# Kernel tuning notes

Measured on AMD Instinct MI355X. Metric: run time of the kernel, lower is better.

## Reference

```python
import jax, jax.numpy as jnp
import numpy as np

B, D_IN, H, C, K, ND = 65536, 1024, 512, 2, 4, 7
LN_EPS = 1e-5
CE_W = jnp.array([0.1, 0.9], dtype=jnp.float32)


def setup_inputs() -> dict:
    key = jax.random.key(0)
    ks = jax.random.split(key, 12)
    x = jax.random.normal(ks[0], (B, D_IN), dtype=jnp.float32)
    labels = jax.random.randint(ks[1], (B,), 0, C)
    domain = jax.random.randint(ks[2], (B,), 0, ND)
    fc1_w = jax.random.normal(ks[3], (120, D_IN), dtype=jnp.float32) / np.sqrt(D_IN)
    fc1_b = jnp.zeros((120,), dtype=jnp.float32)
    fc2_w = jax.random.normal(ks[4], (H, 120), dtype=jnp.float32) / np.sqrt(120)
    fc2_b = jnp.zeros((H,), dtype=jnp.float32)
    ln_g = jnp.ones((H,), dtype=jnp.float32)
    ln_b = jnp.zeros((H,), dtype=jnp.float32)
    sms = 0.1 * jax.random.normal(ks[5], (K + 1, H, C), dtype=jnp.float32)
    sm_biases = 0.1 * jax.random.normal(ks[6], (K + 1, C), dtype=jnp.float32)
    embs = 1e-4 * jax.random.normal(ks[7], (ND, K), dtype=jnp.float32)
    cs_wt = jnp.asarray(0.1, dtype=jnp.float32) + 1e-4 * jax.random.normal(ks[8], (), dtype=jnp.float32)
    return {"x": x, "labels": labels, "domain": domain, "fc1_w": fc1_w, "fc1_b": fc1_b,
            "fc2_w": fc2_w, "fc2_b": fc2_b, "ln_g": ln_g, "ln_b": ln_b,
            "sms": sms, "sm_biases": sm_biases, "embs": embs, "cs_wt": cs_wt}


def _weighted_ce(logits, labels, w):
    # torch CrossEntropyLoss(weight=w): sum_i w[y_i]*nll_i / sum_i w[y_i]
    logp = jax.nn.log_softmax(logits, axis=-1)
    nll = -jnp.take_along_axis(logp, labels[:, None], axis=1)[:, 0]
    wl = w[labels]
    return jnp.sum(wl * nll) / jnp.sum(wl)


def reference(x, labels, domain, fc1_w, fc1_b, fc2_w, fc2_b, ln_g, ln_b, sms, sm_biases, embs, cs_wt):
    h = jax.nn.relu(x @ fc1_w.T + fc1_b)           # [B,120]
    h = jax.nn.relu(h @ fc2_w.T + fc2_b)           # [B,H]
    mu = jnp.mean(h, axis=-1, keepdims=True)
    var = jnp.var(h, axis=-1, keepdims=True)
    h = (h - mu) / jnp.sqrt(var + LN_EPS) * ln_g + ln_b

    # common classifier (expert 0)
    logits_common = h @ sms[0] + sm_biases[0]      # [B,C]

    # domain mixture weights
    dom1h = jax.nn.one_hot(domain, ND, dtype=jnp.float32)
    c_wts = dom1h @ embs                           # [B,K]
    c_wts = jnp.tanh(jnp.concatenate([jnp.full((h.shape[0], 1), 1.0, jnp.float32) * cs_wt, c_wts], axis=1))  # [B,K+1]

    # reordered einsum chain: K+1 small GEMMs then weighted sum (avoids [B,K+1,H] weight tensor)
    per_k = jnp.einsum('bh,khc->bkc', h, sms)      # [B,K+1,C]
    logits_spec = jnp.einsum('bk,bkc->bc', c_wts, per_k) + c_wts @ sm_biases  # [B,C]

    specific_loss = _weighted_ce(logits_spec, labels, CE_W)
    class_loss = _weighted_ce(logits_common, labels, CE_W)

    # orthogonality penalty: per-class gram of expert weight columns vs identity
    cps = jnp.einsum('khc,jhc->ckj', sms, sms)     # [C,K+1,K+1]
    orth_loss = jnp.mean((cps - jnp.eye(K + 1, dtype=jnp.float32)[None]) ** 2)

    loss = class_loss + specific_loss + orth_loss
    return (loss, logits_common, class_loss, specific_loss, orth_loss)
```

## Files before the change

### kernel.cpp

```cpp
#include <hip/hip_runtime.h>
#include <hip/hip_bf16.h>

typedef __attribute__((ext_vector_type(8))) short short8;
typedef __attribute__((ext_vector_type(4))) float floatx4;
typedef __attribute__((ext_vector_type(8))) unsigned short ushort8;

#define BTOT 65536
#define WS_W1BF   0u
#define WS_W2BF   262144u
#define WS_GBF    393216u
#define WS_CONST  409600u
#define WS_H1BF   524288u
#define WS_PART   17301504u

__device__ __forceinline__ unsigned short f2bf(float f) {
  unsigned u = __float_as_uint(f);
  unsigned r = u + 0x7FFFu + ((u >> 16) & 1u);
  return (unsigned short)(r >> 16);
}

__device__ __forceinline__ unsigned cvtpk(float lo, float hi) {
  unsigned r;
  asm("v_cvt_pk_bf16_f32 %0, %1, %2" : "=v"(r) : "v"(lo), "v"(hi));
  return r;
}

__device__ __forceinline__ void gload16(const void* g, void* l) {
  __builtin_amdgcn_global_load_lds(
      (const __attribute__((address_space(1))) unsigned int*)g,
      (__attribute__((address_space(3))) unsigned int*)l, 16, 0, 0);
}

__global__ __launch_bounds__(256) void k0_prep(
    const float* __restrict__ w1, const float* __restrict__ w2,
    const float* __restrict__ ln_g, const float* __restrict__ ln_b,
    const float* __restrict__ sms, const float* __restrict__ smb,
    const float* __restrict__ embs, const float* __restrict__ cs,
    unsigned char* __restrict__ ws) {
  const int blk = blockIdx.x, tid = threadIdx.x;
  if (blk < 32) {
    for (int g = blk * 256 + tid; g < 16384; g += 32 * 256) {
      int ks = g >> 10, d = g & 1023;
      int n = d >> 3, cp = d & 7, c = cp ^ (n & 7);
      ushort8 u;
      if (n < 120) {
        const float* s = w1 + n * 1024 + ks * 64 + c * 8;
        float4 v0 = *(const float4*)s, v1 = *(const float4*)(s + 4);
        u[0] = f2bf(v0.x); u[1] = f2bf(v0.y); u[2] = f2bf(v0.z); u[3] = f2bf(v0.w);
        u[4] = f2bf(v1.x); u[5] = f2bf(v1.y); u[6] = f2bf(v1.z); u[7] = f2bf(v1.w);
      } else {
#pragma unroll
        for (int j = 0; j < 8; ++j) u[j] = 0;
      }
      *(ushort8*)(ws + WS_W1BF + (unsigned)g * 16) = u;
    }
  } else if (blk < 40) {
    for (int g = (blk - 32) * 256 + tid; g < 8192; g += 8 * 256) {
      int lane = g & 63, f = g >> 6;
      int nt = f & 3, ks = (f >> 2) & 3, w = f >> 4;
      int n = w * 64 + nt * 16 + (lane & 15);
      ushort8 u;
#pragma unroll
      for (int j = 0; j < 8; ++j) {
        int khat = ks * 32 + (lane >> 4) * 8 + j;
        int kcol = (khat & 7) * 16 + (khat >> 3);
        u[j] = (kcol < 120) ? f2bf(w2[n * 120 + kcol]) : (unsigned short)0;
      }
      *(ushort8*)(ws + WS_W2BF + (unsigned)g * 16) = u;
    }
  } else if (blk == 40) {
    for (int e = tid; e < 1024; e += 256) {
      int t = e >> 6, lane = e & 63, q = lane & 15;
      ushort8 u;
#pragma unroll
      for (int j = 0; j < 8; ++j) {
        int khat = t * 32 + (lane >> 4) * 8 + j;
        int col = (khat >> 6) * 64 + (khat & 3) * 16 + ((khat >> 2) & 15);
        float v = 0.f;
        if (q < 10) { int kk = q >> 1, c = q & 1; v = ln_g[col] * sms[kk * 1024 + col * 2 + c]; }
        u[j] = f2bf(v);
      }
      *(ushort8*)(ws + WS_GBF + (unsigned)e * 16) = u;
    }
  } else {
    float* cst = (float*)(ws + WS_CONST);
    int lane = tid & 63, w = tid >> 6;
    for (int q = w; q < 10; q += 4) {
      int kk = q >> 1, c = q & 1;
      float s = 0.f;
#pragma unroll
      for (int i = 0; i < 8; ++i) { int k = lane + 64 * i; s += ln_b[k] * sms[kk * 1024 + k * 2 + c]; }
#pragma unroll
      for (int o = 32; o >= 1; o >>= 1) s += __shfl_xor(s, o);
      if (lane == 0) cst[q] = s + smb[kk * 2 + c];
    }
    if (tid == 0) cst[16] = tanhf(cs[0]);
    if (tid < 28) cst[32 + tid] = tanhf(embs[tid]);
  }
}

__global__ __launch_bounds__(512, 4) void k1_gemm1(
    const float* __restrict__ x, const unsigned char* __restrict__ w1bf,
    const float* __restrict__ b1, unsigned char* __restrict__ h1bf) {
  __shared__ unsigned char lds[32768];
  const int tid = threadIdx.x, lane = tid & 63, w = tid >> 6;
  const int l15 = lane & 15, l4 = lane >> 4;

  float b1v[8];
#pragma unroll
  for (int nt = 0; nt < 8; ++nt) {
    int col = nt * 16 + l15;
    b1v[nt] = b1[col < 120 ? col : 119];
  }
  __builtin_amdgcn_sched_barrier(0);

  const float* xbase = x + ((long)blockIdx.x * 128 + w * 16 + l15) * 1024 + l4 * 8;
  const unsigned char* wsrc = w1bf + w * 2048 + lane * 16;

  floatx4 acc[8];
#pragma unroll
  for (int i = 0; i < 8; ++i) acc[i] = floatx4{0.f, 0.f, 0.f, 0.f};

  float4 p[2][4];
  gload16(wsrc, lds + w * 2048);
  gload16(wsrc + 1024, lds + w * 2048 + 1024);
  __builtin_amdgcn_sched_barrier(0);
#pragma unroll
  for (int ss = 0; ss < 2; ++ss) {
    p[0][ss * 2]     = *(const float4*)(xbase + ss * 32);
    p[0][ss * 2 + 1] = *(const float4*)(xbase + ss * 32 + 4);
  }
#pragma unroll
  for (int ss = 0; ss < 2; ++ss) {
    p[1][ss * 2]     = *(const float4*)(xbase + 64 + ss * 32);
    p[1][ss * 2 + 1] = *(const float4*)(xbase + 64 + ss * 32 + 4);
  }
  __builtin_amdgcn_sched_barrier(0);
  asm volatile("s_waitcnt vmcnt(8)" ::: "memory");
  __builtin_amdgcn_s_barrier();

#pragma unroll
  for (int t = 0; t < 16; ++t) {
    const int cur = t & 1;
    short8 afr[2];
#pragma unroll
    for (int ss = 0; ss < 2; ++ss) {
      float4 a0 = p[cur][ss * 2], a1 = p[cur][ss * 2 + 1];
      union { unsigned u[4]; short8 s; } tmp;
      tmp.u[0] = cvtpk(a0.x, a0.y);
      tmp.u[1] = cvtpk(a0.z, a0.w);
      tmp.u[2] = cvtpk(a1.x, a1.y);
      tmp.u[3] = cvtpk(a1.z, a1.w);
      afr[ss] = tmp.s;
    }
    __builtin_amdgcn_sched_barrier(0);
    if (t < 15) {
      gload16(wsrc + (t + 1) * 16384, lds + (cur ^ 1) * 16384 + w * 2048);
      gload16(wsrc + (t + 1) * 16384 + 1024, lds + (cur ^ 1) * 16384 + w * 2048 + 1024);
    }
    __builtin_amdgcn_sched_barrier(0);
    if (t < 14) {
#pragma unroll
      for (int ss = 0; ss < 2; ++ss) {
        p[cur][ss * 2]     = *(const float4*)(xbase + (t + 2) * 64 + ss * 32);
        p[cur][ss * 2 + 1] = *(const float4*)(xbase + (t + 2) * 64 + ss * 32 + 4);
      }
    }
    __builtin_amdgcn_sched_barrier(0);
    const unsigned char* Wc = lds + cur * 16384;
#pragma unroll
    for (int ss = 0; ss < 2; ++ss)
#pragma unroll
      for (int nt = 0; nt < 8; ++nt) {
        int n = nt * 16 + l15;
        short8 b = *(const short8*)(Wc + n * 128 + ((ss * 64 + l4 * 16) ^ ((n & 7) << 4)));
        acc[nt] = __builtin_amdgcn_mfma_f32_16x16x32_bf16(afr[ss], b, acc[nt], 0, 0, 0);
      }
    if (t < 14)       asm volatile("s_waitcnt vmcnt(4) lgkmcnt(0)" ::: "memory");
    else if (t == 14) asm volatile("s_waitcnt vmcnt(0) lgkmcnt(0)" ::: "memory");
    else              asm volatile("s_waitcnt lgkmcnt(0)" ::: "memory");
    __builtin_amdgcn_s_barrier();
  }

#pragma unroll
  for (int r = 0; r < 4; ++r) {
    int row = w * 16 + l4 * 4 + r;
    float v[8];
#pragma unroll
    for (int nt = 0; nt < 8; ++nt) {
      float t0 = acc[nt][r] + b1v[nt];
      v[nt] = t0 > 0.f ? t0 : 0.f;
    }
    if (l15 >= 8) v[7] = 0.f;
    union { unsigned u[4]; short8 s; } tmp;
    tmp.u[0] = cvtpk(v[0], v[1]);
    tmp.u[1] = cvtpk(v[2], v[3]);
    tmp.u[2] = cvtpk(v[4], v[5]);
    tmp.u[3] = cvtpk(v[6], v[7]);
    *(short8*)(lds + row * 256 + ((l15 * 16) ^ ((row & 7) << 4))) = tmp.s;
  }
  __syncthreads();
  {
    const unsigned char* s = lds + tid * 64;
    unsigned char* d = h1bf + (long)blockIdx.x * 32768 + tid * 64;
    *(float4*)(d)      = *(const float4*)(s);
    *(float4*)(d + 16) = *(const float4*)(s + 16);
    *(float4*)(d + 32) = *(const float4*)(s + 32);
    *(float4*)(d + 48) = *(const float4*)(s + 48);
  }
}

__global__ __launch_bounds__(512, 4) void k2_fused(
    const unsigned char* __restrict__ h1bf, const unsigned char* __restrict__ w2f,
    const unsigned char* __restrict__ gbf, const float* __restrict__ cst,
    const float* __restrict__ b2, const int* __restrict__ labels,
    const int* __restrict__ domain, float* __restrict__ out,
    float* __restrict__ partials) {
  extern __shared__ unsigned char lds[];
  unsigned char* h1s = lds;
  unsigned char* h2s = lds;
  float* stats = (float*)(lds + 65536);
  float* musig = (float*)(lds + 70656);
  float* Af    = (float*)(lds + 71168);

  const int tid = threadIdx.x, lane = tid & 63, w = tid >> 6;
  const int l15 = lane & 15, l4 = lane >> 4;
  const long row0 = (long)blockIdx.x * 64;
  const int n0 = w * 64;

  {
    const unsigned char* hs = h1bf + ((long)(blockIdx.x >> 1)) * 32768 +
                              (blockIdx.x & 1) * 16384 + w * 2048 + lane * 16;
    gload16(hs, h1s + w * 2048);
    gload16(hs + 1024, h1s + w * 2048 + 1024);
  }
  float b2v[4];
#pragma unroll
  for (int nt = 0; nt < 4; ++nt) b2v[nt] = b2[n0 + nt * 16 + l15];
  __syncthreads();

  floatx4 acc[4][4];
#pragma unroll
  for (int i = 0; i < 4; ++i)
#pragma unroll
    for (int j = 0; j < 4; ++j) acc[i][j] = floatx4{0.f, 0.f, 0.f, 0.f};
#pragma unroll
  for (int ks = 0; ks < 4; ++ks) {
    short8 a[4], b[4];
#pragma unroll
    for (int nt = 0; nt < 4; ++nt)
      b[nt] = *(const short8*)(w2f + (((w * 4 + ks) * 4 + nt) * 64 + lane) * 16);
#pragma unroll
    for (int mt = 0; mt < 4; ++mt) {
      int r = mt * 16 + l15;
      a[mt] = *(const short8*)(h1s + r * 256 + ((ks * 64 + l4 * 16) ^ ((r & 7) << 4)));
    }
#pragma unroll
    for (int mt = 0; mt < 4; ++mt)
#pragma unroll
      for (int nt = 0; nt < 4; ++nt)
        acc[mt][nt] = __builtin_amdgcn_mfma_f32_16x16x32_bf16(a[mt], b[nt], acc[mt][nt], 0, 0, 0);
  }

#pragma unroll
  for (int mt = 0; mt < 4; ++mt)
#pragma unroll
    for (int nt = 0; nt < 4; ++nt)
#pragma unroll
      for (int r = 0; r < 4; ++r) {
        float v = acc[mt][nt][r] + b2v[nt];
        acc[mt][nt][r] = v > 0.f ? v : 0.f;
      }
#pragma unroll
  for (int mt = 0; mt < 4; ++mt)
#pragma unroll
    for (int r = 0; r < 4; ++r) {
      float s = 0.f, q2 = 0.f;
#pragma unroll
      for (int nt = 0; nt < 4; ++nt) { float v = acc[mt][nt][r]; s += v; q2 += v * v; }
#pragma unroll
      for (int o = 1; o <= 8; o <<= 1) { s += __shfl_xor(s, o); q2 += __shfl_xor(q2, o); }
      if (l15 == 0) {
        int row = mt * 16 + l4 * 4 + r;
        stats[row * 20 + w * 2] = s;
        stats[row * 20 + w * 2 + 1] = q2;
      }
    }
  __syncthreads();

  if (tid < 64) {
    float S = 0.f, Q = 0.f;
#pragma unroll
    for (int j = 0; j < 8; ++j) { S += stats[tid * 20 + j * 2]; Q += stats[tid * 20 + j * 2 + 1]; }
    float mu = S * (1.f / 512.f);
    float var = Q * (1.f / 512.f) - mu * mu;
    musig[tid * 2] = mu;
    musig[tid * 2 + 1] = rsqrtf(var + 1e-5f);
  }
  __syncthreads();

#pragma unroll
  for (int mt = 0; mt < 4; ++mt)
#pragma unroll
    for (int r = 0; r < 4; ++r) {
      int row = mt * 16 + l4 * 4 + r;
      float mu = musig[row * 2], rs = musig[row * 2 + 1];
      uint2 qq;
      qq.x = cvtpk((acc[mt][0][r] - mu) * rs, (acc[mt][1][r] - mu) * rs);
      qq.y = cvtpk((acc[mt][2][r] - mu) * rs, (acc[mt][3][r] - mu) * rs);
      *(uint2*)(h2s + row * 1024 + ((w * 128 + l15 * 8) ^ ((row & 7) << 4))) = qq;
    }
  __syncthreads();

  if (w < 4) {
    floatx4 a3 = floatx4{0.f, 0.f, 0.f, 0.f};
    int row = w * 16 + l15;
#pragma unroll
    for (int t = 0; t < 16; ++t) {
      short8 aa = *(const short8*)(h2s + row * 1024 + ((t * 64 + l4 * 16) ^ ((row & 7) << 4)));
      short8 bb = *(const short8*)(gbf + t * 1024 + lane * 16);
      a3 = __builtin_amdgcn_mfma_f32_16x16x32_bf16(aa, bb, a3, 0, 0, 0);
    }
#pragma unroll
    for (int reg = 0; reg < 4; ++reg) {
      int orow = w * 16 + l4 * 4 + reg;
      if (l15 < 10) Af[orow * 20 + l15] = a3[reg];
    }
  }
  __syncthreads();

  if (tid < 64) {
    long grow = row0 + tid;
    float pd[10];
#pragma unroll
    for (int q = 0; q < 10; ++q) pd[q] = Af[tid * 20 + q] + cst[q];
    int lab = labels[grow], dm = domain[grow];
    float cw0 = cst[16];
    float ls0 = cw0 * pd[0], ls1 = cw0 * pd[1];
#pragma unroll
    for (int kk = 1; kk < 5; ++kk) {
      float c = cst[32 + dm * 4 + kk - 1];
      ls0 += c * pd[kk * 2];
      ls1 += c * pd[kk * 2 + 1];
    }
    float lc0 = pd[0], lc1 = pd[1];
    *(float2*)(out + 1 + grow * 2) = float2{lc0, lc1};
    float m1 = fmaxf(lc0, lc1), n1 = fminf(lc0, lc1);
    float lse1 = m1 + logf(1.f + expf(n1 - m1));
    float nllc = lse1 - (lab ? lc1 : lc0);
    float m2 = fmaxf(ls0, ls1), n2 = fminf(ls0, ls1);
    float lse2 = m2 + logf(1.f + expf(n2 - m2));
    float nlls = lse2 - (lab ? ls1 : ls0);
    float wl = lab ? 0.9f : 0.1f;
    float wsum = wl, scom = wl * nllc, sspec = wl * nlls;
#pragma unroll
    for (int o = 32; o >= 1; o >>= 1) {
      wsum += __shfl_xor(wsum, o);
      scom += __shfl_xor(scom, o);
      sspec += __shfl_xor(sspec, o);
    }
    if (tid == 0) {
      partials[(long)blockIdx.x * 4] = wsum;
      partials[(long)blockIdx.x * 4 + 1] = scom;
      partials[(long)blockIdx.x * 4 + 2] = sspec;
    }
  }
}

__global__ __launch_bounds__(256) void k3_finalize(
    const float* __restrict__ partials, const float* __restrict__ sms,
    float* __restrict__ out) {
  __shared__ float wsums[4][3];
  __shared__ float ow[4];
  const int tid = threadIdx.x;
  const int lane = tid & 63, wid = tid >> 6;
  float sw = 0.f, sc = 0.f, ss = 0.f;
  for (int i = tid; i < 1024; i += 256) {
    sw += partials[i * 4];
    sc += partials[i * 4 + 1];
    ss += partials[i * 4 + 2];
  }
#pragma unroll
  for (int o = 32; o >= 1; o >>= 1) {
    sw += __shfl_xor(sw, o);
    sc += __shfl_xor(sc, o);
    ss += __shfl_xor(ss, o);
  }
  if (lane == 0) { wsums[wid][0] = sw; wsums[wid][1] = sc; wsums[wid][2] = ss; }

  float osum = 0.f;
  for (int p = wid; p < 50; p += 4) {
    int c = p / 25, kk = (p / 5) % 5, j = p % 5;
    float acc = 0.f;
#pragma unroll
    for (int hh = 0; hh < 8; ++hh) {
      int h = lane + 64 * hh;
      acc += sms[kk * 1024 + h * 2 + c] * sms[j * 1024 + h * 2 + c];
    }
#pragma unroll
    for (int o = 32; o >= 1; o >>= 1) acc += __shfl_xor(acc, o);
    float d = acc - ((kk == j) ? 1.f : 0.f);
    osum += d * d;
  }
  if (lane == 0) ow[wid] = osum;
  __syncthreads();
  if (tid == 0) {
    float SW = 0.f, SC = 0.f, SS = 0.f, OS = 0.f;
    for (int w = 0; w < 4; ++w) {
      SW += wsums[w][0]; SC += wsums[w][1]; SS += wsums[w][2]; OS += ow[w];
    }
    float orth = OS * (1.f / 50.f);
    float cls = SC / SW;
    float spec = SS / SW;
    out[0] = cls + spec + orth;
    out[131073] = cls;
    out[131074] = spec;
    out[131075] = orth;
  }
}

extern "C" void kernel_launch(void* const* d_in, const int* in_sizes, int n_in,
                              void* d_out, int out_size, void* d_ws, size_t ws_size,
                              hipStream_t stream) {
  const float* x      = (const float*)d_in[0];
  const int* labels   = (const int*)d_in[1];
  const int* domain   = (const int*)d_in[2];
  const float* fc1_w  = (const float*)d_in[3];
  const float* fc1_b  = (const float*)d_in[4];
  const float* fc2_w  = (const float*)d_in[5];
  const float* fc2_b  = (const float*)d_in[6];
  const float* ln_g   = (const float*)d_in[7];
  const float* ln_b   = (const float*)d_in[8];
  const float* sms    = (const float*)d_in[9];
  const float* sm_b   = (const float*)d_in[10];
  const float* embs   = (const float*)d_in[11];
  const float* cs_wt  = (const float*)d_in[12];
  float* out = (float*)d_out;
  unsigned char* ws = (unsigned char*)d_ws;

  (void)hipFuncSetAttribute((const void*)k2_fused,
                            hipFuncAttributeMaxDynamicSharedMemorySize, 76800);

  hipLaunchKernelGGL(k0_prep, dim3(42), dim3(256), 0, stream,
                     fc1_w, fc2_w, ln_g, ln_b, sms, sm_b, embs, cs_wt, ws);
  hipLaunchKernelGGL(k1_gemm1, dim3(BTOT / 128), dim3(512), 0, stream,
                     x, ws + WS_W1BF, fc1_b, ws + WS_H1BF);
  hipLaunchKernelGGL(k2_fused, dim3(BTOT / 64), dim3(512), 76800, stream,
                     ws + WS_H1BF, ws + WS_W2BF, ws + WS_GBF,
                     (const float*)(ws + WS_CONST), fc2_b,
                     labels, domain, out, (float*)(ws + WS_PART));
  hipLaunchKernelGGL(k3_finalize, dim3(1), dim3(256), 0, stream,
                     (const float*)(ws + WS_PART), sms, out);
}
```

Before: 104.7 us.

## Keep fc1 weights in registers and stream x through double-buffered LDS

The first GEMM kernel becomes a persistent-style kernel with 256 blocks, each covering 256 rows in eight 32-row steps. Each wave loads its 16-column slice of the bf16 fc1 weights into registers once, so weights are no longer re-streamed through LDS for every block. The fp32 x rows are converted to bf16 and staged in a swizzled, double-buffered LDS tile, with the next chunk's global loads overlapping the current chunk's MFMAs. Output is packed and written per chunk, and the downstream kernel's h1 indexing is simplified to match. The cost is heavy register use (128 VGPRs of weights), a large dynamic LDS allocation, and fewer resident waves to hide the latency of x loads.

```diff
diff --git a/kernel.cpp b/kernel.cpp
--- a/kernel.cpp
+++ b/kernel.cpp
@@ -99,114 +99,98 @@
   }
 }
 
-__global__ __launch_bounds__(512, 4) void k1_gemm1(
+__global__ __launch_bounds__(512, 2) void k1_gemm1(
     const float* __restrict__ x, const unsigned char* __restrict__ w1bf,
     const float* __restrict__ b1, unsigned char* __restrict__ h1bf) {
-  __shared__ unsigned char lds[32768];
+  extern __shared__ unsigned char lds[];
+  unsigned char* pack = lds + 131072;
+
   const int tid = threadIdx.x, lane = tid & 63, w = tid >> 6;
   const int l15 = lane & 15, l4 = lane >> 4;
-
-  float b1v[8];
-#pragma unroll
-  for (int nt = 0; nt < 8; ++nt) {
-    int col = nt * 16 + l15;
-    b1v[nt] = b1[col < 120 ? col : 119];
-  }
-  __builtin_amdgcn_sched_barrier(0);
-
-  const float* xbase = x + ((long)blockIdx.x * 128 + w * 16 + l15) * 1024 + l4 * 8;
-  const unsigned char* wsrc = w1bf + w * 2048 + lane * 16;
-
-  floatx4 acc[8];
-#pragma unroll
-  for (int i = 0; i < 8; ++i) acc[i] = floatx4{0.f, 0.f, 0.f, 0.f};
-
-  float4 p[2][4];
-  gload16(wsrc, lds + w * 2048);
-  gload16(wsrc + 1024, lds + w * 2048 + 1024);
-  __builtin_amdgcn_sched_barrier(0);
-#pragma unroll
-  for (int ss = 0; ss < 2; ++ss) {
-    p[0][ss * 2]     = *(const float4*)(xbase + ss * 32);
-    p[0][ss * 2 + 1] = *(const float4*)(xbase + ss * 32 + 4);
-  }
-#pragma unroll
-  for (int ss = 0; ss < 2; ++ss) {
-    p[1][ss * 2]     = *(const float4*)(xbase + 64 + ss * 32);
-    p[1][ss * 2 + 1] = *(const float4*)(xbase + 64 + ss * 32 + 4);
-  }
-  __builtin_amdgcn_sched_barrier(0);
-  asm volatile("s_waitcnt vmcnt(8)" ::: "memory");
+  const int n = w * 16 + l15;
+  const float bias = b1[n < 120 ? n : 119];
+
+  short8 bf[32];
+#pragma unroll
+  for (int f = 0; f < 32; ++f) {
+    int ks = f >> 1, ss = f & 1;
+    bf[f] = *(const short8*)(w1bf + ks * 16384 + n * 128 +
+                             ((ss * 64 + l4 * 16) ^ ((n & 7) << 4)));
+  }
+
+  const long xrowbase = (long)blockIdx.x * 256;
+  const int srow = tid >> 8;
+  const int scol = (tid & 255) * 4;
+
+  float4 st[16];
+  {
+    const float* src = x + xrowbase * 1024 + (long)tid * 4;
+#pragma unroll
+    for (int i = 0; i < 16; ++i) st[i] = *(const float4*)(src + i * 2048);
+#pragma unroll
+    for (int i = 0; i < 16; ++i) {
+      int row = i * 2 + srow;
+      unsigned off = (unsigned)(row * 2048 + (((scol >> 3) * 16) ^ ((row & 7) << 4)) + (scol & 7) * 2);
+      uint2 q;
+      q.x = cvtpk(st[i].x, st[i].y);
+      q.y = cvtpk(st[i].z, st[i].w);
+      *(uint2*)(lds + off) = q;
+    }
+  }
+  asm volatile("s_waitcnt lgkmcnt(0)" ::: "memory");
   __builtin_amdgcn_s_barrier();
 
-#pragma unroll
-  for (int t = 0; t < 16; ++t) {
-    const int cur = t & 1;
-    short8 afr[2];
-#pragma unroll
-    for (int ss = 0; ss < 2; ++ss) {
-      float4 a0 = p[cur][ss * 2], a1 = p[cur][ss * 2 + 1];
-      union { unsigned u[4]; short8 s; } tmp;
-      tmp.u[0] = cvtpk(a0.x, a0.y);
-      tmp.u[1] = cvtpk(a0.z, a0.w);
-      tmp.u[2] = cvtpk(a1.x, a1.y);
-      tmp.u[3] = cvtpk(a1.z, a1.w);
-      afr[ss] = tmp.s;
+  for (int s = 0; s < 8; ++s) {
+    const int cur = s & 1;
+    if (s < 7) {
+      const float* src = x + (xrowbase + (s + 1) * 32) * 1024 + (long)tid * 4;
+#pragma unroll
+      for (int i = 0; i < 16; ++i) st[i] = *(const float4*)(src + i * 2048);
     }
     __builtin_amdgcn_sched_barrier(0);
-    if (t < 15) {
-      gload16(wsrc + (t + 1) * 16384, lds + (cur ^ 1) * 16384 + w * 2048);
-      gload16(wsrc + (t + 1) * 16384 + 1024, lds + (cur ^ 1) * 16384 + w * 2048 + 1024);
+    floatx4 acc0 = floatx4{0.f, 0.f, 0.f, 0.f};
+    floatx4 acc1 = floatx4{0.f, 0.f, 0.f, 0.f};
+    const unsigned char* Xc = lds + cur * 65536;
+    const unsigned abase = (unsigned)(l15 * 2048);
+#pragma unroll
+    for (int kk = 0; kk < 32; ++kk) {
+      unsigned ko = (unsigned)((kk * 64 + l4 * 16) ^ ((l15 & 7) << 4));
+      short8 a0 = *(const short8*)(Xc + abase + ko);
+      short8 a1 = *(const short8*)(Xc + abase + 32768 + ko);
+      acc0 = __builtin_amdgcn_mfma_f32_16x16x32_bf16(a0, bf[kk], acc0, 0, 0, 0);
+      acc1 = __builtin_amdgcn_mfma_f32_16x16x32_bf16(a1, bf[kk], acc1, 0, 0, 0);
     }
     __builtin_amdgcn_sched_barrier(0);
-    if (t < 14) {
-#pragma unroll
-      for (int ss = 0; ss < 2; ++ss) {
-        p[cur][ss * 2]     = *(const float4*)(xbase + (t + 2) * 64 + ss * 32);
-        p[cur][ss * 2 + 1] = *(const float4*)(xbase + (t + 2) * 64 + ss * 32 + 4);
-      }
-    }
-    __builtin_amdgcn_sched_barrier(0);
-    const unsigned char* Wc = lds + cur * 16384;
-#pragma unroll
-    for (int ss = 0; ss < 2; ++ss)
-#pragma unroll
-      for (int nt = 0; nt < 8; ++nt) {
-        int n = nt * 16 + l15;
-        short8 b = *(const short8*)(Wc + n * 128 + ((ss * 64 + l4 * 16) ^ ((n & 7) << 4)));
-        acc[nt] = __builtin_amdgcn_mfma_f32_16x16x32_bf16(afr[ss], b, acc[nt], 0, 0, 0);
-      }
-    if (t < 14)       asm volatile("s_waitcnt vmcnt(4) lgkmcnt(0)" ::: "memory");
-    else if (t == 14) asm volatile("s_waitcnt vmcnt(0) lgkmcnt(0)" ::: "memory");
-    else              asm volatile("s_waitcnt lgkmcnt(0)" ::: "memory");
+    if (s < 7) {
+      unsigned char* base = lds + (cur ^ 1) * 65536;
+#pragma unroll
+      for (int i = 0; i < 16; ++i) {
+        int row = i * 2 + srow;
+        unsigned off = (unsigned)(row * 2048 + (((scol >> 3) * 16) ^ ((row & 7) << 4)) + (scol & 7) * 2);
+        uint2 q;
+        q.x = cvtpk(st[i].x, st[i].y);
+        q.y = cvtpk(st[i].z, st[i].w);
+        *(uint2*)(base + off) = q;
+      }
+    }
+#pragma unroll
+    for (int mt = 0; mt < 2; ++mt)
+#pragma unroll
+      for (int r = 0; r < 4; ++r) {
+        int row = mt * 16 + l4 * 4 + r;
+        float v = (mt ? acc1[r] : acc0[r]) + bias;
+        v = v > 0.f ? v : 0.f;
+        if (n >= 120) v = 0.f;
+        *(unsigned short*)(pack + row * 256 + ((l15 * 16) ^ ((row & 7) << 4)) + w * 2) = f2bf(v);
+      }
+    asm volatile("s_waitcnt lgkmcnt(0)" ::: "memory");
     __builtin_amdgcn_s_barrier();
-  }
-
-#pragma unroll
-  for (int r = 0; r < 4; ++r) {
-    int row = w * 16 + l4 * 4 + r;
-    float v[8];
-#pragma unroll
-    for (int nt = 0; nt < 8; ++nt) {
-      float t0 = acc[nt][r] + b1v[nt];
-      v[nt] = t0 > 0.f ? t0 : 0.f;
-    }
-    if (l15 >= 8) v[7] = 0.f;
-    union { unsigned u[4]; short8 s; } tmp;
-    tmp.u[0] = cvtpk(v[0], v[1]);
-    tmp.u[1] = cvtpk(v[2], v[3]);
-    tmp.u[2] = cvtpk(v[4], v[5]);
-    tmp.u[3] = cvtpk(v[6], v[7]);
-    *(short8*)(lds + row * 256 + ((l15 * 16) ^ ((row & 7) << 4))) = tmp.s;
-  }
-  __syncthreads();
-  {
-    const unsigned char* s = lds + tid * 64;
-    unsigned char* d = h1bf + (long)blockIdx.x * 32768 + tid * 64;
-    *(float4*)(d)      = *(const float4*)(s);
-    *(float4*)(d + 16) = *(const float4*)(s + 16);
-    *(float4*)(d + 32) = *(const float4*)(s + 32);
-    *(float4*)(d + 48) = *(const float4*)(s + 48);
+    {
+      float4 q = *(const float4*)(pack + tid * 16);
+      *(float4*)(h1bf + (xrowbase + s * 32) * 256 + tid * 16) = q;
+    }
+    asm volatile("s_waitcnt lgkmcnt(0)" ::: "memory");
+    __builtin_amdgcn_s_barrier();
   }
 }
 
@@ -229,8 +213,7 @@
   const int n0 = w * 64;
 
   {
-    const unsigned char* hs = h1bf + ((long)(blockIdx.x >> 1)) * 32768 +
-                              (blockIdx.x & 1) * 16384 + w * 2048 + lane * 16;
+    const unsigned char* hs = h1bf + (long)blockIdx.x * 16384 + w * 2048 + lane * 16;
     gload16(hs, h1s + w * 2048);
     gload16(hs + 1024, h1s + w * 2048 + 1024);
   }
@@ -438,12 +421,14 @@
   float* out = (float*)d_out;
   unsigned char* ws = (unsigned char*)d_ws;
 
+  (void)hipFuncSetAttribute((const void*)k1_gemm1,
+                            hipFuncAttributeMaxDynamicSharedMemorySize, 139264);
   (void)hipFuncSetAttribute((const void*)k2_fused,
                             hipFuncAttributeMaxDynamicSharedMemorySize, 76800);
 
   hipLaunchKernelGGL(k0_prep, dim3(42), dim3(256), 0, stream,
                      fc1_w, fc2_w, ln_g, ln_b, sms, sm_b, embs, cs_wt, ws);
-  hipLaunchKernelGGL(k1_gemm1, dim3(BTOT / 128), dim3(512), 0, stream,
+  hipLaunchKernelGGL(k1_gemm1, dim3(256), dim3(512), 139264, stream,
                      x, ws + WS_W1BF, fc1_b, ws + WS_H1BF);
   hipLaunchKernelGGL(k2_fused, dim3(BTOT / 64), dim3(512), 76800, stream,
                      ws + WS_H1BF, ws + WS_W2BF, ws + WS_GBF,
```

Measured after the change: 123.4 us. 1.18x slower.

## Fuse first GEMM with second GEMM, layernorm and loss stages into one kernel

Applied to the files above, without the earlier changes.

Merges the fc1 GEMM kernel with the fc2/layernorm/classifier/loss kernel so the 128-row bf16 hidden tile stays in LDS instead of going through a 16 MB global buffer. Each block now processes its 128 rows as two 64-row halves. The classifier GEMM is staged through a 32 KB LDS region in four column chunks, which adds extra barriers. Fewer blocks and more serialized work per block may reduce parallelism and latency hiding, in exchange for removing the global round trip and one kernel launch.

```diff
diff --git a/kernel.cpp b/kernel.cpp
--- a/kernel.cpp
+++ b/kernel.cpp
@@ -10,8 +10,7 @@
 #define WS_W2BF   262144u
 #define WS_GBF    393216u
 #define WS_CONST  409600u
-#define WS_H1BF   524288u
-#define WS_PART   17301504u
+#define WS_PART   524288u
 
 __device__ __forceinline__ unsigned short f2bf(float f) {
   unsigned u = __float_as_uint(f);
@@ -99,10 +98,18 @@
   }
 }
 
-__global__ __launch_bounds__(512, 4) void k1_gemm1(
+__global__ __launch_bounds__(512, 4) void kf_fused(
     const float* __restrict__ x, const unsigned char* __restrict__ w1bf,
-    const float* __restrict__ b1, unsigned char* __restrict__ h1bf) {
-  __shared__ unsigned char lds[32768];
+    const float* __restrict__ b1, const unsigned char* __restrict__ w2f,
+    const unsigned char* __restrict__ gbf, const float* __restrict__ cst,
+    const float* __restrict__ b2, const int* __restrict__ labels,
+    const int* __restrict__ domain, float* __restrict__ out,
+    float* __restrict__ partials) {
+  extern __shared__ unsigned char lds[];
+  float* stats = (float*)(lds + 49152);
+  float* musig = (float*)(lds + 54272);
+  float* Af    = (float*)(lds + 54784);
+
   const int tid = threadIdx.x, lane = tid & 63, w = tid >> 6;
   const int l15 = lane & 15, l4 = lane >> 4;
 
@@ -117,9 +124,9 @@
   const float* xbase = x + ((long)blockIdx.x * 128 + w * 16 + l15) * 1024 + l4 * 8;
   const unsigned char* wsrc = w1bf + w * 2048 + lane * 16;
 
-  floatx4 acc[8];
-#pragma unroll
-  for (int i = 0; i < 8; ++i) acc[i] = floatx4{0.f, 0.f, 0.f, 0.f};
+  floatx4 acc1[8];
+#pragma unroll
+  for (int i = 0; i < 8; ++i) acc1[i] = floatx4{0.f, 0.f, 0.f, 0.f};
 
   float4 p[2][4];
   gload16(wsrc, lds + w * 2048);
@@ -174,7 +181,7 @@
       for (int nt = 0; nt < 8; ++nt) {
         int n = nt * 16 + l15;
         short8 b = *(const short8*)(Wc + n * 128 + ((ss * 64 + l4 * 16) ^ ((n & 7) << 4)));
-        acc[nt] = __builtin_amdgcn_mfma_f32_16x16x32_bf16(afr[ss], b, acc[nt], 0, 0, 0);
+        acc1[nt] = __builtin_amdgcn_mfma_f32_16x16x32_bf16(afr[ss], b, acc1[nt], 0, 0, 0);
       }
     if (t < 14)       asm volatile("s_waitcnt vmcnt(4) lgkmcnt(0)" ::: "memory");
     else if (t == 14) asm volatile("s_waitcnt vmcnt(0) lgkmcnt(0)" ::: "memory");
@@ -188,7 +195,7 @@
     float v[8];
 #pragma unroll
     for (int nt = 0; nt < 8; ++nt) {
-      float t0 = acc[nt][r] + b1v[nt];
+      float t0 = acc1[nt][r] + b1v[nt];
       v[nt] = t0 > 0.f ? t0 : 0.f;
     }
     if (l15 >= 8) v[7] = 0.f;
@@ -200,169 +207,154 @@
     *(short8*)(lds + row * 256 + ((l15 * 16) ^ ((row & 7) << 4))) = tmp.s;
   }
   __syncthreads();
-  {
-    const unsigned char* s = lds + tid * 64;
-    unsigned char* d = h1bf + (long)blockIdx.x * 32768 + tid * 64;
-    *(float4*)(d)      = *(const float4*)(s);
-    *(float4*)(d + 16) = *(const float4*)(s + 16);
-    *(float4*)(d + 32) = *(const float4*)(s + 32);
-    *(float4*)(d + 48) = *(const float4*)(s + 48);
-  }
-}
-
-__global__ __launch_bounds__(512, 4) void k2_fused(
-    const unsigned char* __restrict__ h1bf, const unsigned char* __restrict__ w2f,
-    const unsigned char* __restrict__ gbf, const float* __restrict__ cst,
-    const float* __restrict__ b2, const int* __restrict__ labels,
-    const int* __restrict__ domain, float* __restrict__ out,
-    float* __restrict__ partials) {
-  extern __shared__ unsigned char lds[];
-  unsigned char* h1s = lds;
-  unsigned char* h2s = lds;
-  float* stats = (float*)(lds + 65536);
-  float* musig = (float*)(lds + 70656);
-  float* Af    = (float*)(lds + 71168);
-
-  const int tid = threadIdx.x, lane = tid & 63, w = tid >> 6;
-  const int l15 = lane & 15, l4 = lane >> 4;
-  const long row0 = (long)blockIdx.x * 64;
+
   const int n0 = w * 64;
-
-  {
-    const unsigned char* hs = h1bf + ((long)(blockIdx.x >> 1)) * 32768 +
-                              (blockIdx.x & 1) * 16384 + w * 2048 + lane * 16;
-    gload16(hs, h1s + w * 2048);
-    gload16(hs + 1024, h1s + w * 2048 + 1024);
-  }
   float b2v[4];
 #pragma unroll
   for (int nt = 0; nt < 4; ++nt) b2v[nt] = b2[n0 + nt * 16 + l15];
-  __syncthreads();
-
-  floatx4 acc[4][4];
-#pragma unroll
-  for (int i = 0; i < 4; ++i)
-#pragma unroll
-    for (int j = 0; j < 4; ++j) acc[i][j] = floatx4{0.f, 0.f, 0.f, 0.f};
-#pragma unroll
-  for (int ks = 0; ks < 4; ++ks) {
-    short8 a[4], b[4];
-#pragma unroll
-    for (int nt = 0; nt < 4; ++nt)
-      b[nt] = *(const short8*)(w2f + (((w * 4 + ks) * 4 + nt) * 64 + lane) * 16);
-#pragma unroll
-    for (int mt = 0; mt < 4; ++mt) {
-      int r = mt * 16 + l15;
-      a[mt] = *(const short8*)(h1s + r * 256 + ((ks * 64 + l4 * 16) ^ ((r & 7) << 4)));
+  float wsumA = 0.f, scomA = 0.f, sspecA = 0.f;
+
+  for (int h = 0; h < 2; ++h) {
+    floatx4 acc[4][4];
+#pragma unroll
+    for (int i = 0; i < 4; ++i)
+#pragma unroll
+      for (int j = 0; j < 4; ++j) acc[i][j] = floatx4{0.f, 0.f, 0.f, 0.f};
+#pragma unroll
+    for (int ks = 0; ks < 4; ++ks) {
+      short8 a[4], b[4];
+#pragma unroll
+      for (int nt = 0; nt < 4; ++nt)
+        b[nt] = *(const short8*)(w2f + (((w * 4 + ks) * 4 + nt) * 64 + lane) * 16);
+#pragma unroll
+      for (int mt = 0; mt < 4; ++mt) {
+        int r = h * 64 + mt * 16 + l15;
+        a[mt] = *(const short8*)(lds + r * 256 + ((ks * 64 + l4 * 16) ^ ((l15 & 7) << 4)));
+      }
+#pragma unroll
+      for (int mt = 0; mt < 4; ++mt)
+#pragma unroll
+        for (int nt = 0; nt < 4; ++nt)
+          acc[mt][nt] = __builtin_amdgcn_mfma_f32_16x16x32_bf16(a[mt], b[nt], acc[mt][nt], 0, 0, 0);
     }
 #pragma unroll
     for (int mt = 0; mt < 4; ++mt)
 #pragma unroll
       for (int nt = 0; nt < 4; ++nt)
-        acc[mt][nt] = __builtin_amdgcn_mfma_f32_16x16x32_bf16(a[mt], b[nt], acc[mt][nt], 0, 0, 0);
-  }
-
-#pragma unroll
-  for (int mt = 0; mt < 4; ++mt)
-#pragma unroll
-    for (int nt = 0; nt < 4; ++nt)
+#pragma unroll
+        for (int r = 0; r < 4; ++r) {
+          float v = acc[mt][nt][r] + b2v[nt];
+          acc[mt][nt][r] = v > 0.f ? v : 0.f;
+        }
+#pragma unroll
+    for (int mt = 0; mt < 4; ++mt)
 #pragma unroll
       for (int r = 0; r < 4; ++r) {
-        float v = acc[mt][nt][r] + b2v[nt];
-        acc[mt][nt][r] = v > 0.f ? v : 0.f;
-      }
-#pragma unroll
-  for (int mt = 0; mt < 4; ++mt)
-#pragma unroll
-    for (int r = 0; r < 4; ++r) {
-      float s = 0.f, q2 = 0.f;
-#pragma unroll
-      for (int nt = 0; nt < 4; ++nt) { float v = acc[mt][nt][r]; s += v; q2 += v * v; }
-#pragma unroll
-      for (int o = 1; o <= 8; o <<= 1) { s += __shfl_xor(s, o); q2 += __shfl_xor(q2, o); }
-      if (l15 == 0) {
-        int row = mt * 16 + l4 * 4 + r;
-        stats[row * 20 + w * 2] = s;
-        stats[row * 20 + w * 2 + 1] = q2;
-      }
-    }
-  __syncthreads();
+        float s = 0.f, q2 = 0.f;
+#pragma unroll
+        for (int nt = 0; nt < 4; ++nt) { float v = acc[mt][nt][r]; s += v; q2 += v * v; }
+#pragma unroll
+        for (int o = 1; o <= 8; o <<= 1) { s += __shfl_xor(s, o); q2 += __shfl_xor(q2, o); }
+        if (l15 == 0) {
+          int rl = mt * 16 + l4 * 4 + r;
+          stats[rl * 20 + w * 2] = s;
+          stats[rl * 20 + w * 2 + 1] = q2;
+        }
+      }
+    __syncthreads();
+    if (tid < 64) {
+      float S = 0.f, Q = 0.f;
+#pragma unroll
+      for (int j = 0; j < 8; ++j) { S += stats[tid * 20 + j * 2]; Q += stats[tid * 20 + j * 2 + 1]; }
+      float mu = S * (1.f / 512.f);
+      float var = Q * (1.f / 512.f) - mu * mu;
+      musig[tid * 2] = mu;
+      musig[tid * 2 + 1] = rsqrtf(var + 1e-5f);
+    }
+    __syncthreads();
+
+    floatx4 a3 = floatx4{0.f, 0.f, 0.f, 0.f};
+#pragma unroll
+    for (int cc = 0; cc < 4; ++cc) {
+      if ((w >> 1) == cc) {
+#pragma unroll
+        for (int mt = 0; mt < 4; ++mt)
+#pragma unroll
+          for (int r = 0; r < 4; ++r) {
+            int rl = mt * 16 + l4 * 4 + r;
+            float mu = musig[rl * 2], rs = musig[rl * 2 + 1];
+            uint2 qq;
+            qq.x = cvtpk((acc[mt][0][r] - mu) * rs, (acc[mt][1][r] - mu) * rs);
+            qq.y = cvtpk((acc[mt][2][r] - mu) * rs, (acc[mt][3][r] - mu) * rs);
+            *(uint2*)(lds + 32768 + rl * 256 +
+                      (((w & 1) * 128 + l15 * 8) ^ ((rl & 7) << 4))) = qq;
+          }
+      }
+      __syncthreads();
+      if (w < 4) {
+        int row = w * 16 + l15;
+#pragma unroll
+        for (int tl = 0; tl < 4; ++tl) {
+          int t = cc * 4 + tl;
+          short8 aa = *(const short8*)(lds + 32768 + row * 256 +
+                                       ((tl * 64 + l4 * 16) ^ ((row & 7) << 4)));
+          short8 bb = *(const short8*)(gbf + t * 1024 + lane * 16);
+          a3 = __builtin_amdgcn_mfma_f32_16x16x32_bf16(aa, bb, a3, 0, 0, 0);
+        }
+      }
+      __syncthreads();
+    }
+    if (w < 4) {
+#pragma unroll
+      for (int reg = 0; reg < 4; ++reg) {
+        int orow = w * 16 + l4 * 4 + reg;
+        if (l15 < 10) Af[orow * 20 + l15] = a3[reg];
+      }
+    }
+    __syncthreads();
+
+    if (tid < 64) {
+      long grow = (long)blockIdx.x * 128 + h * 64 + tid;
+      float pd[10];
+#pragma unroll
+      for (int q = 0; q < 10; ++q) pd[q] = Af[tid * 20 + q] + cst[q];
+      int lab = labels[grow], dm = domain[grow];
+      float cw0 = cst[16];
+      float ls0 = cw0 * pd[0], ls1 = cw0 * pd[1];
+#pragma unroll
+      for (int kk = 1; kk < 5; ++kk) {
+        float c = cst[32 + dm * 4 + kk - 1];
+        ls0 += c * pd[kk * 2];
+        ls1 += c * pd[kk * 2 + 1];
+      }
+      float lc0 = pd[0], lc1 = pd[1];
+      out[1 + grow * 2 + 0] = lc0;
+      out[1 + grow * 2 + 1] = lc1;
+      float m1 = fmaxf(lc0, lc1), nn1 = fminf(lc0, lc1);
+      float lse1 = m1 + logf(1.f + expf(nn1 - m1));
+      float nllc = lse1 - (lab ? lc1 : lc0);
+      float m2 = fmaxf(ls0, ls1), nn2 = fminf(ls0, ls1);
+      float lse2 = m2 + logf(1.f + expf(nn2 - m2));
+      float nlls = lse2 - (lab ? ls1 : ls0);
+      float wl = lab ? 0.9f : 0.1f;
+      wsumA += wl;
+      scomA += wl * nllc;
+      sspecA += wl * nlls;
+    }
+    __syncthreads();
+  }
 
   if (tid < 64) {
-    float S = 0.f, Q = 0.f;
-#pragma unroll
-    for (int j = 0; j < 8; ++j) { S += stats[tid * 20 + j * 2]; Q += stats[tid * 20 + j * 2 + 1]; }
-    float mu = S * (1.f / 512.f);
-    float var = Q * (1.f / 512.f) - mu * mu;
-    musig[tid * 2] = mu;
-    musig[tid * 2 + 1] = rsqrtf(var + 1e-5f);
-  }
-  __syncthreads();
-
-#pragma unroll
-  for (int mt = 0; mt < 4; ++mt)
-#pragma unroll
-    for (int r = 0; r < 4; ++r) {
-      int row = mt * 16 + l4 * 4 + r;
-      float mu = musig[row * 2], rs = musig[row * 2 + 1];
-      uint2 qq;
-      qq.x = cvtpk((acc[mt][0][r] - mu) * rs, (acc[mt][1][r] - mu) * rs);
-      qq.y = cvtpk((acc[mt][2][r] - mu) * rs, (acc[mt][3][r] - mu) * rs);
-      *(uint2*)(h2s + row * 1024 + ((w * 128 + l15 * 8) ^ ((row & 7) << 4))) = qq;
-    }
-  __syncthreads();
-
-  if (w < 4) {
-    floatx4 a3 = floatx4{0.f, 0.f, 0.f, 0.f};
-    int row = w * 16 + l15;
-#pragma unroll
-    for (int t = 0; t < 16; ++t) {
-      short8 aa = *(const short8*)(h2s + row * 1024 + ((t * 64 + l4 * 16) ^ ((row & 7) << 4)));
-      short8 bb = *(const short8*)(gbf + t * 1024 + lane * 16);
-      a3 = __builtin_amdgcn_mfma_f32_16x16x32_bf16(aa, bb, a3, 0, 0, 0);
-    }
-#pragma unroll
-    for (int reg = 0; reg < 4; ++reg) {
-      int orow = w * 16 + l4 * 4 + reg;
-      if (l15 < 10) Af[orow * 20 + l15] = a3[reg];
-    }
-  }
-  __syncthreads();
-
-  if (tid < 64) {
-    long grow = row0 + tid;
-    float pd[10];
-#pragma unroll
-    for (int q = 0; q < 10; ++q) pd[q] = Af[tid * 20 + q] + cst[q];
-    int lab = labels[grow], dm = domain[grow];
-    float cw0 = cst[16];
-    float ls0 = cw0 * pd[0], ls1 = cw0 * pd[1];
-#pragma unroll
-    for (int kk = 1; kk < 5; ++kk) {
-      float c = cst[32 + dm * 4 + kk - 1];
-      ls0 += c * pd[kk * 2];
-      ls1 += c * pd[kk * 2 + 1];
-    }
-    float lc0 = pd[0], lc1 = pd[1];
-    *(float2*)(out + 1 + grow * 2) = float2{lc0, lc1};
-    float m1 = fmaxf(lc0, lc1), n1 = fminf(lc0, lc1);
-    float lse1 = m1 + logf(1.f + expf(n1 - m1));
-    float nllc = lse1 - (lab ? lc1 : lc0);
-    float m2 = fmaxf(ls0, ls1), n2 = fminf(ls0, ls1);
-    float lse2 = m2 + logf(1.f + expf(n2 - m2));
-    float nlls = lse2 - (lab ? ls1 : ls0);
-    float wl = lab ? 0.9f : 0.1f;
-    float wsum = wl, scom = wl * nllc, sspec = wl * nlls;
 #pragma unroll
     for (int o = 32; o >= 1; o >>= 1) {
-      wsum += __shfl_xor(wsum, o);
-      scom += __shfl_xor(scom, o);
-      sspec += __shfl_xor(sspec, o);
+      wsumA += __shfl_xor(wsumA, o);
+      scomA += __shfl_xor(scomA, o);
+      sspecA += __shfl_xor(sspecA, o);
     }
     if (tid == 0) {
-      partials[(long)blockIdx.x * 4] = wsum;
-      partials[(long)blockIdx.x * 4 + 1] = scom;
-      partials[(long)blockIdx.x * 4 + 2] = sspec;
+      partials[(long)blockIdx.x * 4]     = wsumA;
+      partials[(long)blockIdx.x * 4 + 1] = scomA;
+      partials[(long)blockIdx.x * 4 + 2] = sspecA;
     }
   }
 }
@@ -375,7 +367,7 @@
   const int tid = threadIdx.x;
   const int lane = tid & 63, wid = tid >> 6;
   float sw = 0.f, sc = 0.f, ss = 0.f;
-  for (int i = tid; i < 1024; i += 256) {
+  for (int i = tid; i < 512; i += 256) {
     sw += partials[i * 4];
     sc += partials[i * 4 + 1];
     ss += partials[i * 4 + 2];
@@ -438,15 +430,13 @@
   float* out = (float*)d_out;
   unsigned char* ws = (unsigned char*)d_ws;
 
-  (void)hipFuncSetAttribute((const void*)k2_fused,
-                            hipFuncAttributeMaxDynamicSharedMemorySize, 76800);
+  (void)hipFuncSetAttribute((const void*)kf_fused,
+                            hipFuncAttributeMaxDynamicSharedMemorySize, 59904);
 
   hipLaunchKernelGGL(k0_prep, dim3(42), dim3(256), 0, stream,
                      fc1_w, fc2_w, ln_g, ln_b, sms, sm_b, embs, cs_wt, ws);
-  hipLaunchKernelGGL(k1_gemm1, dim3(BTOT / 128), dim3(512), 0, stream,
-                     x, ws + WS_W1BF, fc1_b, ws + WS_H1BF);
-  hipLaunchKernelGGL(k2_fused, dim3(BTOT / 64), dim3(512), 76800, stream,
-                     ws + WS_H1BF, ws + WS_W2BF, ws + WS_GBF,
+  hipLaunchKernelGGL(kf_fused, dim3(BTOT / 128), dim3(512), 59904, stream,
+                     x, ws + WS_W1BF, fc1_b, ws + WS_W2BF, ws + WS_GBF,
                      (const float*)(ws + WS_CONST), fc2_b,
                      labels, domain, out, (float*)(ws + WS_PART));
   hipLaunchKernelGGL(k3_finalize, dim3(1), dim3(256), 0, stream,
```

New measurement: 217.1 us. +107.2%, slower.
